# Kernel optimization log

Measured on AMD Instinct MI355X. Metric: run time of the kernel, lower is better.

## Reference

```python
import jax, jax.numpy as jnp
import numpy as np

B_SZ, C_IN, C_OUT, H, W = 16, 32, 32, 128, 128
K, CODE, PAD, FACTOR = 3, 2, 1, 1.0

def setup_inputs() -> dict:
    key = jax.random.key(0)
    ks = jax.random.split(key, 7)
    s = 0.05
    return {
        "x": jax.random.normal(ks[0], (B_SZ, C_IN, H, W), jnp.float32),
        "codes": jax.random.normal(ks[1], (B_SZ, CODE, CODE), jnp.float32),
        "weight": jax.random.normal(ks[2], (C_OUT, C_IN, K, K), jnp.float32) * s,
        "A": jax.random.normal(ks[3], (C_IN, CODE, K, K), jnp.float32) * s,
        "Bm": jax.random.normal(ks[4], (C_OUT, CODE, K, K), jnp.float32) * s,
        "bias": jax.random.normal(ks[5], (C_OUT,), jnp.float32) * s,
        "bias_context": jax.random.normal(ks[6], (CODE, C_OUT), jnp.float32) * s,
    }

def reference(x, codes, weight, A, Bm, bias, bias_context):
    # hypernetwork weight synthesis: [b, out, in, k, k]
    w_ctx = jnp.einsum('ickl,bcr->birkl', A, codes)            # [b, in, code, k, k]
    w_ctx = jnp.einsum('birkl,orkl->boikl', w_ctx, Bm)         # [b, out, in, k, k]
    combined_weight = weight[None] + FACTOR * w_ctx
    # per-sample bias from diagonal of codes
    diag = jnp.diagonal(codes, axis1=-2, axis2=-1)             # [b, code]
    combined_bias = bias[None] + FACTOR * (diag @ bias_context)  # [b, out]
    # circular padding then per-sample VALID conv (== unfold + einsum)
    xp = jnp.pad(x, ((0, 0), (0, 0), (PAD, PAD), (PAD, PAD)), mode='wrap')
    def conv_one(xi, wi):
        return jax.lax.conv_general_dilated(
            xi[None], wi, window_strides=(1, 1), padding='VALID',
            dimension_numbers=('NCHW', 'OIHW', 'NCHW'))[0]
    out = jax.vmap(conv_one)(xp, combined_weight)              # [b, out, H, W]
    return out + combined_bias[:, :, None, None]
```

## Files before the change

### kernel.cpp

```cpp
#include <hip/hip_runtime.h>

typedef short bf16x8 __attribute__((ext_vector_type(8)));
typedef float f32x4  __attribute__((ext_vector_type(4)));
typedef unsigned short u16;
typedef unsigned int   u32;

#define HH 128
#define WW 128

__device__ __forceinline__ u32 cvt_pk_bf16(float lo, float hi) {
    u32 r;
    asm volatile("v_cvt_pk_bf16_f32 %0, %1, %2" : "=v"(r) : "v"(lo), "v"(hi));
    return r;
}

__global__ __launch_bounds__(512, 1) void geps_mfma_kernel(
    const float* __restrict__ x, const float* __restrict__ codes,
    const float* __restrict__ weight, const float* __restrict__ A,
    const float* __restrict__ Bm, const float* __restrict__ bias,
    const float* __restrict__ bctx, float* __restrict__ out)
{
    __shared__ bf16x8 lds_x[3072];
    __shared__ bf16x8 lds_w[1152];
    __shared__ float  lds_ctx[576];
    __shared__ float  lds_b[32];

    const int tid  = threadIdx.x;
    const int l    = tid & 63;
    const int wvid = tid >> 6;
    const int row  = wvid >> 1;
    const int nh   = wvid & 1;

    const int orig = blockIdx.x;
    const int vb   = (orig & 7) * 32 + (orig >> 3);
    const int b    = vb >> 4;
    const int grp  = vb & 15;
    const int h0   = grp * 8;

    const float c00 = codes[b * 4 + 0];
    const float c01 = codes[b * 4 + 1];
    const float c10 = codes[b * 4 + 2];
    const float c11 = codes[b * 4 + 3];

    for (int j = tid; j < 576; j += 512) {
        int i = j / 18, rem = j % 18, r = rem / 9, kl = rem % 9;
        float a0 = A[(i * 2 + 0) * 9 + kl];
        float a1 = A[(i * 2 + 1) * 9 + kl];
        lds_ctx[j] = (r == 0) ? (a0 * c00 + a1 * c10) : (a0 * c01 + a1 * c11);
    }
    if (tid < 32) lds_b[tid] = bias[tid] + c00 * bctx[tid] + c11 * bctx[32 + tid];
    __syncthreads();

    for (int j = tid; j < 1152; j += 512) {
        int kl = j >> 7, rem = j & 127, o = rem >> 2, kb = rem & 3;
        float m0 = Bm[(o * 2 + 0) * 9 + kl];
        float m1 = Bm[(o * 2 + 1) * 9 + kl];
        float wf[8];
        #pragma unroll
        for (int jj = 0; jj < 8; ++jj) {
            int i = kb * 8 + jj;
            wf[jj] = weight[(o * 32 + i) * 9 + kl]
                   + lds_ctx[i * 18 + kl] * m0
                   + lds_ctx[i * 18 + 9 + kl] * m1;
        }
        u32 pk[4];
        #pragma unroll
        for (int q = 0; q < 4; ++q) pk[q] = cvt_pk_bf16(wf[2 * q], wf[2 * q + 1]);
        *(uint4*)&lds_w[kl * 128 + (o >> 4) * 64 + kb * 16 + (o & 15)] =
            make_uint4(pk[0], pk[1], pk[2], pk[3]);
    }

    #pragma unroll
    for (int it = 0; it < 3; ++it) {
        int idx = it * 512 + tid;
        int cp  = idx & 63;
        int ig  = (idx >> 6) & 3;
        int rr  = idx >> 8;
        int c0  = cp * 2;
        int grow = (h0 - 1 + rr) & 127;
        const float* src = x + ((size_t)(b * 32 + ig * 8) * HH + grow) * WW + c0;
        float2 f[8];
        #pragma unroll
        for (int jj = 0; jj < 8; ++jj)
            f[jj] = *(const float2*)(src + (size_t)jj * HH * WW);
        u32 p0[4], p1[4];
        #pragma unroll
        for (int q = 0; q < 4; ++q) {
            p0[q] = cvt_pk_bf16(f[2 * q].x, f[2 * q + 1].x);
            p1[q] = cvt_pk_bf16(f[2 * q].y, f[2 * q + 1].y);
        }
        int didx = rr * 512 + (c0 >> 4) * 64 + ig * 16 + (c0 & 15);
        *(uint4*)&lds_x[didx]     = make_uint4(p0[0], p0[1], p0[2], p0[3]);
        *(uint4*)&lds_x[didx + 1] = make_uint4(p1[0], p1[1], p1[2], p1[3]);
    }
    __syncthreads();

    const int awb = (l >> 4) * 16 + (l & 15);
    bf16x8 af[9][2];
    #pragma unroll
    for (int kl = 0; kl < 9; ++kl)
        #pragma unroll
        for (int oh = 0; oh < 2; ++oh)
            af[kl][oh] = lds_w[kl * 128 + oh * 64 + awb];

    const int p = l & 15, igf = l >> 4;
    int bb[3];
    #pragma unroll
    for (int dl = -1; dl <= 1; ++dl) {
        int pq = p + dl;
        bb[dl + 1] = (pq & 15) + ((pq >> 4) << 6) + igf * 16;
    }

    float blr[2][4];
    #pragma unroll
    for (int oh = 0; oh < 2; ++oh)
        #pragma unroll
        for (int r = 0; r < 4; ++r)
            blr[oh][r] = lds_b[oh * 16 + (l >> 4) * 4 + r];

    auto compute_store = [&](int s0, int s1, int s2, int h) {
        f32x4 acc[2][4];
        #pragma unroll
        for (int oh = 0; oh < 2; ++oh)
            #pragma unroll
            for (int q = 0; q < 4; ++q) acc[oh][q] = (f32x4){0.f, 0.f, 0.f, 0.f};
        const int sl[3] = {s0, s1, s2};
        #pragma unroll
        for (int q = 0; q < 4; ++q) {
            const int nt = nh * 4 + q;
            #pragma unroll
            for (int lc = 0; lc < 3; ++lc) {
                int t = (bb[lc] + nt * 64) & 511;
                #pragma unroll
                for (int k = 0; k < 3; ++k) {
                    bf16x8 bfv = lds_x[sl[k] * 512 + t];
                    acc[0][q] = __builtin_amdgcn_mfma_f32_16x16x32_bf16(
                        af[k * 3 + lc][0], bfv, acc[0][q], 0, 0, 0);
                    acc[1][q] = __builtin_amdgcn_mfma_f32_16x16x32_bf16(
                        af[k * 3 + lc][1], bfv, acc[1][q], 0, 0, 0);
                }
            }
        }
        const size_t obase =
            ((size_t)(b * 32 + (l >> 4) * 4) * HH + h) * WW + p;
        #pragma unroll
        for (int oh = 0; oh < 2; ++oh)
            #pragma unroll
            for (int q = 0; q < 4; ++q)
                #pragma unroll
                for (int r = 0; r < 4; ++r)
                    out[obase + (size_t)(oh * 16 + r) * (HH * WW) + (nh * 4 + q) * 16] =
                        acc[oh][q][r] + blr[oh][r];
    };

    float2 pf[16];
    #pragma unroll
    for (int it = 0; it < 2; ++it) {
        int idx = it * 512 + tid;
        int cp  = idx & 63;
        int ig  = (idx >> 6) & 3;
        int rr  = idx >> 8;
        int grow = (h0 + 5 + rr) & 127;
        const float* src = x + ((size_t)(b * 32 + ig * 8) * HH + grow) * WW + cp * 2;
        #pragma unroll
        for (int jj = 0; jj < 8; ++jj)
            pf[it * 8 + jj] = *(const float2*)(src + (size_t)jj * HH * WW);
    }

    compute_store(row, row + 1, row + 2, h0 + row);

    __syncthreads();

    #pragma unroll
    for (int it = 0; it < 2; ++it) {
        int idx = it * 512 + tid;
        int cp  = idx & 63;
        int ig  = (idx >> 6) & 3;
        int rr  = idx >> 8;
        int c0  = cp * 2;
        u32 p0[4], p1[4];
        #pragma unroll
        for (int q = 0; q < 4; ++q) {
            p0[q] = cvt_pk_bf16(pf[it * 8 + 2 * q].x, pf[it * 8 + 2 * q + 1].x);
            p1[q] = cvt_pk_bf16(pf[it * 8 + 2 * q].y, pf[it * 8 + 2 * q + 1].y);
        }
        int didx = rr * 512 + (c0 >> 4) * 64 + ig * 16 + (c0 & 15);
        *(uint4*)&lds_x[didx]     = make_uint4(p0[0], p0[1], p0[2], p0[3]);
        *(uint4*)&lds_x[didx + 1] = make_uint4(p1[0], p1[1], p1[2], p1[3]);
    }
    __syncthreads();

    {
        int r0 = 4 + row, r1 = 5 + row, r2 = 6 + row;
        compute_store(r0 >= 6 ? r0 - 6 : r0,
                      r1 >= 6 ? r1 - 6 : r1,
                      r2 >= 6 ? r2 - 6 : r2,
                      h0 + 4 + row);
    }
}

extern "C" void kernel_launch(void* const* d_in, const int* in_sizes, int n_in,
                              void* d_out, int out_size, void* d_ws, size_t ws_size,
                              hipStream_t stream) {
    const float* x      = (const float*)d_in[0];
    const float* codes  = (const float*)d_in[1];
    const float* weight = (const float*)d_in[2];
    const float* A      = (const float*)d_in[3];
    const float* Bm     = (const float*)d_in[4];
    const float* bias   = (const float*)d_in[5];
    const float* bctx   = (const float*)d_in[6];
    float* out = (float*)d_out;

    hipLaunchKernelGGL(geps_mfma_kernel, dim3(256), dim3(512), 0, stream,
                       x, codes, weight, A, Bm, bias, bctx, out);
}
```

Baseline: 23.54 us.

## Use 1024-thread blocks covering all eight rows in a single pass

Doubles the block size to 1024 threads so each of 16 waves computes one output row at once. The whole 10-row input halo is staged into shared memory up front, replacing the two-phase prefetch-and-reload ring buffer. The x staging is issued before the weight synthesis so those global loads overlap. The second half of the A fragments is now read from LDS inside the loop to save registers. This gives more waves per CU for latency hiding, at the cost of losing the software-pipelined overlap of the second tile load with compute, more LDS use, and a tighter register budget per thread.

After: 23.73 us. About the same (+0.8%).

```diff
diff --git a/kernel.cpp b/kernel.cpp
--- a/kernel.cpp
+++ b/kernel.cpp
@@ -14,13 +14,13 @@
     return r;
 }
 
-__global__ __launch_bounds__(512, 1) void geps_mfma_kernel(
+__global__ __launch_bounds__(1024, 1) void geps_mfma_kernel(
     const float* __restrict__ x, const float* __restrict__ codes,
     const float* __restrict__ weight, const float* __restrict__ A,
     const float* __restrict__ Bm, const float* __restrict__ bias,
     const float* __restrict__ bctx, float* __restrict__ out)
 {
-    __shared__ bf16x8 lds_x[3072];
+    __shared__ bf16x8 lds_x[5120];
     __shared__ bf16x8 lds_w[1152];
     __shared__ float  lds_ctx[576];
     __shared__ float  lds_b[32];
@@ -42,7 +42,8 @@
     const float c10 = codes[b * 4 + 2];
     const float c11 = codes[b * 4 + 3];
 
-    for (int j = tid; j < 576; j += 512) {
+    if (tid < 576) {
+        int j = tid;
         int i = j / 18, rem = j % 18, r = rem / 9, kl = rem % 9;
         float a0 = A[(i * 2 + 0) * 9 + kl];
         float a1 = A[(i * 2 + 1) * 9 + kl];
@@ -51,7 +52,32 @@
     if (tid < 32) lds_b[tid] = bias[tid] + c00 * bctx[tid] + c11 * bctx[32 + tid];
     __syncthreads();
 
-    for (int j = tid; j < 1152; j += 512) {
+    #pragma unroll
+    for (int it = 0; it < 5; ++it) {
+        int idx   = it * 1024 + tid;
+        int jh    = idx & 1;
+        int cp    = (idx >> 1) & 63;
+        int ig    = (idx >> 7) & 3;
+        int rr    = idx >> 9;
+        int c0    = cp * 2;
+        int grow  = (h0 - 1 + rr) & 127;
+        const float* src =
+            x + ((size_t)(b * 32 + ig * 8 + jh * 4) * HH + grow) * WW + c0;
+        float2 f[4];
+        #pragma unroll
+        for (int jj = 0; jj < 4; ++jj)
+            f[jj] = *(const float2*)(src + (size_t)jj * HH * WW);
+        u32 w0a = cvt_pk_bf16(f[0].x, f[1].x);
+        u32 w0b = cvt_pk_bf16(f[2].x, f[3].x);
+        u32 w1a = cvt_pk_bf16(f[0].y, f[1].y);
+        u32 w1b = cvt_pk_bf16(f[2].y, f[3].y);
+        int didx = rr * 512 + (c0 >> 4) * 64 + ig * 16 + (c0 & 15);
+        u32* base = (u32*)lds_x;
+        *(uint2*)&base[didx * 4 + jh * 2]       = make_uint2(w0a, w0b);
+        *(uint2*)&base[(didx + 1) * 4 + jh * 2] = make_uint2(w1a, w1b);
+    }
+
+    for (int j = tid; j < 1152; j += 1024) {
         int kl = j >> 7, rem = j & 127, o = rem >> 2, kb = rem & 3;
         float m0 = Bm[(o * 2 + 0) * 9 + kl];
         float m1 = Bm[(o * 2 + 1) * 9 + kl];
@@ -69,39 +95,13 @@
         *(uint4*)&lds_w[kl * 128 + (o >> 4) * 64 + kb * 16 + (o & 15)] =
             make_uint4(pk[0], pk[1], pk[2], pk[3]);
     }
-
-    #pragma unroll
-    for (int it = 0; it < 3; ++it) {
-        int idx = it * 512 + tid;
-        int cp  = idx & 63;
-        int ig  = (idx >> 6) & 3;
-        int rr  = idx >> 8;
-        int c0  = cp * 2;
-        int grow = (h0 - 1 + rr) & 127;
-        const float* src = x + ((size_t)(b * 32 + ig * 8) * HH + grow) * WW + c0;
-        float2 f[8];
-        #pragma unroll
-        for (int jj = 0; jj < 8; ++jj)
-            f[jj] = *(const float2*)(src + (size_t)jj * HH * WW);
-        u32 p0[4], p1[4];
-        #pragma unroll
-        for (int q = 0; q < 4; ++q) {
-            p0[q] = cvt_pk_bf16(f[2 * q].x, f[2 * q + 1].x);
-            p1[q] = cvt_pk_bf16(f[2 * q].y, f[2 * q + 1].y);
-        }
-        int didx = rr * 512 + (c0 >> 4) * 64 + ig * 16 + (c0 & 15);
-        *(uint4*)&lds_x[didx]     = make_uint4(p0[0], p0[1], p0[2], p0[3]);
-        *(uint4*)&lds_x[didx + 1] = make_uint4(p1[0], p1[1], p1[2], p1[3]);
-    }
     __syncthreads();
 
     const int awb = (l >> 4) * 16 + (l & 15);
-    bf16x8 af[9][2];
+    bf16x8 af0[9];
     #pragma unroll
     for (int kl = 0; kl < 9; ++kl)
-        #pragma unroll
-        for (int oh = 0; oh < 2; ++oh)
-            af[kl][oh] = lds_w[kl * 128 + oh * 64 + awb];
+        af0[kl] = lds_w[kl * 128 + awb];
 
     const int p = l & 15, igf = l >> 4;
     int bb[3];
@@ -111,6 +111,30 @@
         bb[dl + 1] = (pq & 15) + ((pq >> 4) << 6) + igf * 16;
     }
 
+    f32x4 acc[2][4];
+    #pragma unroll
+    for (int oh = 0; oh < 2; ++oh)
+        #pragma unroll
+        for (int q = 0; q < 4; ++q) acc[oh][q] = (f32x4){0.f, 0.f, 0.f, 0.f};
+
+    #pragma unroll
+    for (int lc = 0; lc < 3; ++lc) {
+        #pragma unroll
+        for (int k = 0; k < 3; ++k) {
+            const bf16x8 a0 = af0[k * 3 + lc];
+            const bf16x8 a1 = lds_w[(k * 3 + lc) * 128 + 64 + awb];
+            #pragma unroll
+            for (int q = 0; q < 4; ++q) {
+                int t = (bb[lc] + (nh * 4 + q) * 64) & 511;
+                bf16x8 bfv = lds_x[(row + k) * 512 + t];
+                acc[0][q] = __builtin_amdgcn_mfma_f32_16x16x32_bf16(
+                    a0, bfv, acc[0][q], 0, 0, 0);
+                acc[1][q] = __builtin_amdgcn_mfma_f32_16x16x32_bf16(
+                    a1, bfv, acc[1][q], 0, 0, 0);
+            }
+        }
+    }
+
     float blr[2][4];
     #pragma unroll
     for (int oh = 0; oh < 2; ++oh)
@@ -118,85 +142,16 @@
         for (int r = 0; r < 4; ++r)
             blr[oh][r] = lds_b[oh * 16 + (l >> 4) * 4 + r];
 
-    auto compute_store = [&](int s0, int s1, int s2, int h) {
-        f32x4 acc[2][4];
+    const int h = h0 + row;
+    const size_t obase = ((size_t)(b * 32 + (l >> 4) * 4) * HH + h) * WW + p;
+    #pragma unroll
+    for (int oh = 0; oh < 2; ++oh)
         #pragma unroll
-        for (int oh = 0; oh < 2; ++oh)
+        for (int q = 0; q < 4; ++q)
             #pragma unroll
-            for (int q = 0; q < 4; ++q) acc[oh][q] = (f32x4){0.f, 0.f, 0.f, 0.f};
-        const int sl[3] = {s0, s1, s2};
-        #pragma unroll
-        for (int q = 0; q < 4; ++q) {
-            const int nt = nh * 4 + q;
-            #pragma unroll
-            for (int lc = 0; lc < 3; ++lc) {
-                int t = (bb[lc] + nt * 64) & 511;
-                #pragma unroll
-                for (int k = 0; k < 3; ++k) {
-                    bf16x8 bfv = lds_x[sl[k] * 512 + t];
-                    acc[0][q] = __builtin_amdgcn_mfma_f32_16x16x32_bf16(
-                        af[k * 3 + lc][0], bfv, acc[0][q], 0, 0, 0);
-                    acc[1][q] = __builtin_amdgcn_mfma_f32_16x16x32_bf16(
-                        af[k * 3 + lc][1], bfv, acc[1][q], 0, 0, 0);
-                }
-            }
-        }
-        const size_t obase =
-            ((size_t)(b * 32 + (l >> 4) * 4) * HH + h) * WW + p;
-        #pragma unroll
-        for (int oh = 0; oh < 2; ++oh)
-            #pragma unroll
-            for (int q = 0; q < 4; ++q)
-                #pragma unroll
-                for (int r = 0; r < 4; ++r)
-                    out[obase + (size_t)(oh * 16 + r) * (HH * WW) + (nh * 4 + q) * 16] =
-                        acc[oh][q][r] + blr[oh][r];
-    };
-
-    float2 pf[16];
-    #pragma unroll
-    for (int it = 0; it < 2; ++it) {
-        int idx = it * 512 + tid;
-        int cp  = idx & 63;
-        int ig  = (idx >> 6) & 3;
-        int rr  = idx >> 8;
-        int grow = (h0 + 5 + rr) & 127;
-        const float* src = x + ((size_t)(b * 32 + ig * 8) * HH + grow) * WW + cp * 2;
-        #pragma unroll
-        for (int jj = 0; jj < 8; ++jj)
-            pf[it * 8 + jj] = *(const float2*)(src + (size_t)jj * HH * WW);
-    }
-
-    compute_store(row, row + 1, row + 2, h0 + row);
-
-    __syncthreads();
-
-    #pragma unroll
-    for (int it = 0; it < 2; ++it) {
-        int idx = it * 512 + tid;
-        int cp  = idx & 63;
-        int ig  = (idx >> 6) & 3;
-        int rr  = idx >> 8;
-        int c0  = cp * 2;
-        u32 p0[4], p1[4];
-        #pragma unroll
-        for (int q = 0; q < 4; ++q) {
-            p0[q] = cvt_pk_bf16(pf[it * 8 + 2 * q].x, pf[it * 8 + 2 * q + 1].x);
-            p1[q] = cvt_pk_bf16(pf[it * 8 + 2 * q].y, pf[it * 8 + 2 * q + 1].y);
-        }
-        int didx = rr * 512 + (c0 >> 4) * 64 + ig * 16 + (c0 & 15);
-        *(uint4*)&lds_x[didx]     = make_uint4(p0[0], p0[1], p0[2], p0[3]);
-        *(uint4*)&lds_x[didx + 1] = make_uint4(p1[0], p1[1], p1[2], p1[3]);
-    }
-    __syncthreads();
-
-    {
-        int r0 = 4 + row, r1 = 5 + row, r2 = 6 + row;
-        compute_store(r0 >= 6 ? r0 - 6 : r0,
-                      r1 >= 6 ? r1 - 6 : r1,
-                      r2 >= 6 ? r2 - 6 : r2,
-                      h0 + 4 + row);
-    }
+            for (int r = 0; r < 4; ++r)
+                out[obase + (size_t)(oh * 16 + r) * (HH * WW) + (nh * 4 + q) * 16] =
+                    acc[oh][q][r] + blr[oh][r];
 }
 
 extern "C" void kernel_launch(void* const* d_in, const int* in_sizes, int n_in,
@@ -211,6 +166,6 @@
     const float* bctx   = (const float*)d_in[6];
     float* out = (float*)d_out;
 
-    hipLaunchKernelGGL(geps_mfma_kernel, dim3(256), dim3(512), 0, stream,
+    hipLaunchKernelGGL(geps_mfma_kernel, dim3(256), dim3(1024), 0, stream,
                        x, codes, weight, A, Bm, bias, bctx, out);
 }
```

## Pipeline row halo loads through six-slot LDS ring with finer wave split

Applied to the files above, without the earlier changes.

Replaces the two-phase compute (four rows, then reload, then four rows) with four stages of two output rows each. Each stage prefetches the next two input rows from global memory into registers, computes, then writes them into a six-slot rolling LDS ring. Waves are now split into four column quarters instead of two halves, and the initial load shrinks from six rows to four. The weight synthesis now overlaps with the x staging, barriers use a lighter waitcnt-plus-s_barrier, and output stores become nontemporal. The aim is to hide global load latency behind MFMA work and shorten the startup before compute, at the cost of more barriers.

Result: no change. 23.72 us (+0.8%).

```diff
diff --git a/kernel.cpp b/kernel.cpp
--- a/kernel.cpp
+++ b/kernel.cpp
@@ -2,8 +2,7 @@
 
 typedef short bf16x8 __attribute__((ext_vector_type(8)));
 typedef float f32x4  __attribute__((ext_vector_type(4)));
-typedef unsigned short u16;
-typedef unsigned int   u32;
+typedef unsigned int u32;
 
 #define HH 128
 #define WW 128
@@ -12,6 +11,12 @@
     u32 r;
     asm volatile("v_cvt_pk_bf16_f32 %0, %1, %2" : "=v"(r) : "v"(lo), "v"(hi));
     return r;
+}
+
+__device__ __forceinline__ void lds_barrier() {
+    asm volatile("s_waitcnt lgkmcnt(0)" ::: "memory");
+    __builtin_amdgcn_s_barrier();
+    __builtin_amdgcn_sched_barrier(0);
 }
 
 __global__ __launch_bounds__(512, 1) void geps_mfma_kernel(
@@ -28,8 +33,8 @@
     const int tid  = threadIdx.x;
     const int l    = tid & 63;
     const int wvid = tid >> 6;
-    const int row  = wvid >> 1;
-    const int nh   = wvid & 1;
+    const int row  = wvid >> 2;
+    const int nq   = wvid & 3;
 
     const int orig = blockIdx.x;
     const int vb   = (orig & 7) * 32 + (orig >> 3);
@@ -49,29 +54,10 @@
         lds_ctx[j] = (r == 0) ? (a0 * c00 + a1 * c10) : (a0 * c01 + a1 * c11);
     }
     if (tid < 32) lds_b[tid] = bias[tid] + c00 * bctx[tid] + c11 * bctx[32 + tid];
-    __syncthreads();
-
-    for (int j = tid; j < 1152; j += 512) {
-        int kl = j >> 7, rem = j & 127, o = rem >> 2, kb = rem & 3;
-        float m0 = Bm[(o * 2 + 0) * 9 + kl];
-        float m1 = Bm[(o * 2 + 1) * 9 + kl];
-        float wf[8];
-        #pragma unroll
-        for (int jj = 0; jj < 8; ++jj) {
-            int i = kb * 8 + jj;
-            wf[jj] = weight[(o * 32 + i) * 9 + kl]
-                   + lds_ctx[i * 18 + kl] * m0
-                   + lds_ctx[i * 18 + 9 + kl] * m1;
-        }
-        u32 pk[4];
-        #pragma unroll
-        for (int q = 0; q < 4; ++q) pk[q] = cvt_pk_bf16(wf[2 * q], wf[2 * q + 1]);
-        *(uint4*)&lds_w[kl * 128 + (o >> 4) * 64 + kb * 16 + (o & 15)] =
-            make_uint4(pk[0], pk[1], pk[2], pk[3]);
-    }
-
-    #pragma unroll
-    for (int it = 0; it < 3; ++it) {
+    lds_barrier();
+
+    #pragma unroll
+    for (int it = 0; it < 2; ++it) {
         int idx = it * 512 + tid;
         int cp  = idx & 63;
         int ig  = (idx >> 6) & 3;
@@ -93,7 +79,26 @@
         *(uint4*)&lds_x[didx]     = make_uint4(p0[0], p0[1], p0[2], p0[3]);
         *(uint4*)&lds_x[didx + 1] = make_uint4(p1[0], p1[1], p1[2], p1[3]);
     }
-    __syncthreads();
+
+    for (int j = tid; j < 1152; j += 512) {
+        int kl = j >> 7, rem = j & 127, o = rem >> 2, kb = rem & 3;
+        float m0 = Bm[(o * 2 + 0) * 9 + kl];
+        float m1 = Bm[(o * 2 + 1) * 9 + kl];
+        float wf[8];
+        #pragma unroll
+        for (int jj = 0; jj < 8; ++jj) {
+            int i = kb * 8 + jj;
+            wf[jj] = weight[(o * 32 + i) * 9 + kl]
+                   + lds_ctx[i * 18 + kl] * m0
+                   + lds_ctx[i * 18 + 9 + kl] * m1;
+        }
+        u32 pk[4];
+        #pragma unroll
+        for (int q = 0; q < 4; ++q) pk[q] = cvt_pk_bf16(wf[2 * q], wf[2 * q + 1]);
+        *(uint4*)&lds_w[kl * 128 + (o >> 4) * 64 + kb * 16 + (o & 15)] =
+            make_uint4(pk[0], pk[1], pk[2], pk[3]);
+    }
+    lds_barrier();
 
     const int awb = (l >> 4) * 16 + (l & 15);
     bf16x8 af[9][2];
@@ -118,84 +123,77 @@
         for (int r = 0; r < 4; ++r)
             blr[oh][r] = lds_b[oh * 16 + (l >> 4) * 4 + r];
 
-    auto compute_store = [&](int s0, int s1, int s2, int h) {
-        f32x4 acc[2][4];
+    const size_t obase0 = (size_t)(b * 32 + (l >> 4) * 4) * (HH * WW) + p;
+
+    #pragma unroll
+    for (int c = 0; c < 4; ++c) {
+        float2 pf[8];
+        int pcp = 0, pig = 0, prr = 0;
+        if (c < 3) {
+            int idx = tid;
+            pcp = idx & 63;
+            pig = (idx >> 6) & 3;
+            prr = 4 + 2 * c + (idx >> 8);
+            int grow = (h0 - 1 + prr) & 127;
+            const float* src =
+                x + ((size_t)(b * 32 + pig * 8) * HH + grow) * WW + pcp * 2;
+            #pragma unroll
+            for (int jj = 0; jj < 8; ++jj)
+                pf[jj] = *(const float2*)(src + (size_t)jj * HH * WW);
+        }
+
+        f32x4 acc[2][2];
         #pragma unroll
         for (int oh = 0; oh < 2; ++oh)
             #pragma unroll
-            for (int q = 0; q < 4; ++q) acc[oh][q] = (f32x4){0.f, 0.f, 0.f, 0.f};
-        const int sl[3] = {s0, s1, s2};
-        #pragma unroll
-        for (int q = 0; q < 4; ++q) {
-            const int nt = nh * 4 + q;
-            #pragma unroll
-            for (int lc = 0; lc < 3; ++lc) {
-                int t = (bb[lc] + nt * 64) & 511;
+            for (int q = 0; q < 2; ++q) acc[oh][q] = (f32x4){0.f, 0.f, 0.f, 0.f};
+
+        const int hr = 2 * c + row;
+        #pragma unroll
+        for (int lc = 0; lc < 3; ++lc) {
+            #pragma unroll
+            for (int k = 0; k < 3; ++k) {
+                int s = hr + k; s = (s >= 6) ? s - 6 : s;
+                const bf16x8 a0 = af[k * 3 + lc][0];
+                const bf16x8 a1 = af[k * 3 + lc][1];
                 #pragma unroll
-                for (int k = 0; k < 3; ++k) {
-                    bf16x8 bfv = lds_x[sl[k] * 512 + t];
+                for (int q = 0; q < 2; ++q) {
+                    int t = (bb[lc] + (nq * 2 + q) * 64) & 511;
+                    bf16x8 bfv = lds_x[s * 512 + t];
                     acc[0][q] = __builtin_amdgcn_mfma_f32_16x16x32_bf16(
-                        af[k * 3 + lc][0], bfv, acc[0][q], 0, 0, 0);
+                        a0, bfv, acc[0][q], 0, 0, 0);
                     acc[1][q] = __builtin_amdgcn_mfma_f32_16x16x32_bf16(
-                        af[k * 3 + lc][1], bfv, acc[1][q], 0, 0, 0);
+                        a1, bfv, acc[1][q], 0, 0, 0);
                 }
             }
         }
-        const size_t obase =
-            ((size_t)(b * 32 + (l >> 4) * 4) * HH + h) * WW + p;
+
+        const size_t ob = obase0 + (size_t)(h0 + hr) * WW;
         #pragma unroll
         for (int oh = 0; oh < 2; ++oh)
             #pragma unroll
-            for (int q = 0; q < 4; ++q)
+            for (int q = 0; q < 2; ++q)
                 #pragma unroll
                 for (int r = 0; r < 4; ++r)
-                    out[obase + (size_t)(oh * 16 + r) * (HH * WW) + (nh * 4 + q) * 16] =
-                        acc[oh][q][r] + blr[oh][r];
-    };
-
-    float2 pf[16];
-    #pragma unroll
-    for (int it = 0; it < 2; ++it) {
-        int idx = it * 512 + tid;
-        int cp  = idx & 63;
-        int ig  = (idx >> 6) & 3;
-        int rr  = idx >> 8;
-        int grow = (h0 + 5 + rr) & 127;
-        const float* src = x + ((size_t)(b * 32 + ig * 8) * HH + grow) * WW + cp * 2;
-        #pragma unroll
-        for (int jj = 0; jj < 8; ++jj)
-            pf[it * 8 + jj] = *(const float2*)(src + (size_t)jj * HH * WW);
-    }
-
-    compute_store(row, row + 1, row + 2, h0 + row);
-
-    __syncthreads();
-
-    #pragma unroll
-    for (int it = 0; it < 2; ++it) {
-        int idx = it * 512 + tid;
-        int cp  = idx & 63;
-        int ig  = (idx >> 6) & 3;
-        int rr  = idx >> 8;
-        int c0  = cp * 2;
-        u32 p0[4], p1[4];
-        #pragma unroll
-        for (int q = 0; q < 4; ++q) {
-            p0[q] = cvt_pk_bf16(pf[it * 8 + 2 * q].x, pf[it * 8 + 2 * q + 1].x);
-            p1[q] = cvt_pk_bf16(pf[it * 8 + 2 * q].y, pf[it * 8 + 2 * q + 1].y);
-        }
-        int didx = rr * 512 + (c0 >> 4) * 64 + ig * 16 + (c0 & 15);
-        *(uint4*)&lds_x[didx]     = make_uint4(p0[0], p0[1], p0[2], p0[3]);
-        *(uint4*)&lds_x[didx + 1] = make_uint4(p1[0], p1[1], p1[2], p1[3]);
-    }
-    __syncthreads();
-
-    {
-        int r0 = 4 + row, r1 = 5 + row, r2 = 6 + row;
-        compute_store(r0 >= 6 ? r0 - 6 : r0,
-                      r1 >= 6 ? r1 - 6 : r1,
-                      r2 >= 6 ? r2 - 6 : r2,
-                      h0 + 4 + row);
+                    __builtin_nontemporal_store(
+                        acc[oh][q][r] + blr[oh][r],
+                        &out[ob + (size_t)(oh * 16 + r) * (HH * WW) +
+                             (nq * 2 + q) * 16]);
+
+        if (c < 3) {
+            u32 p0[4], p1[4];
+            #pragma unroll
+            for (int q = 0; q < 4; ++q) {
+                p0[q] = cvt_pk_bf16(pf[2 * q].x, pf[2 * q + 1].x);
+                p1[q] = cvt_pk_bf16(pf[2 * q].y, pf[2 * q + 1].y);
+            }
+            int wslot = (prr >= 6) ? prr - 6 : prr;
+            int c0 = pcp * 2;
+            int didx = wslot * 512 + (c0 >> 4) * 64 + pig * 16 + (c0 & 15);
+            *(uint4*)&lds_x[didx]     = make_uint4(p0[0], p0[1], p0[2], p0[3]);
+            *(uint4*)&lds_x[didx + 1] = make_uint4(p1[0], p1[1], p1[2], p1[3]);
+            lds_barrier();
+        }
     }
 }
 
```
